# Optimization experiments

Hardware: AMD Instinct MI355X
Metric: run time of the kernel (lower is better)

## Reference

```python
import jax, jax.numpy as jnp
import numpy as np

B, T, D = 2, 2048, 1024
H = 16
HD = D // H  # 64


def setup_inputs() -> dict:
    key = jax.random.key(0)
    k1, k2, k3, k4, k5 = jax.random.split(key, 5)
    s = 0.02
    return {
        "x": jax.random.normal(k1, (B, T, D), dtype=jnp.float32),
        "Wqkv": jax.random.normal(k2, (D, 3 * D), dtype=jnp.float32) * s,
        "bqkv": jax.random.normal(k3, (3 * D,), dtype=jnp.float32) * s,
        "Wout": jax.random.normal(k4, (D, D), dtype=jnp.float32) * s,
        "bout": jax.random.normal(k5, (D,), dtype=jnp.float32) * s,
    }


def reference(x, Wqkv, bqkv, Wout, bout):
    b, t, c = x.shape
    qkv = (x @ Wqkv + bqkv).reshape(b, t, 3, H, HD)
    q = jnp.transpose(qkv[:, :, 0], (0, 2, 1, 3))  # [B,H,T,HD]
    k = jnp.transpose(qkv[:, :, 1], (0, 2, 1, 3))
    v = jnp.transpose(qkv[:, :, 2], (0, 2, 1, 3))
    att = jnp.einsum("bhqd,bhkd->bhqk", q, k) * (HD ** -0.5)
    mask = jnp.tril(jnp.ones((t, t), dtype=bool))  # causal, no past kv
    att = jnp.where(mask, att, -jnp.inf)
    att = jax.nn.softmax(att, axis=-1)
    y = jnp.einsum("bhqk,bhkd->bhqd", att, v)
    y = jnp.transpose(y, (0, 2, 1, 3)).reshape(b, t, c)
    return y @ Wout + bout
```

## Files before the change

kernel.cpp:

```cpp
#include <hip/hip_runtime.h>
#include <hip/hip_bf16.h>
#include <math.h>

#define B_  2
#define T_  2048
#define D_  1024
#define H_  16
#define HD_ 64

typedef __attribute__((ext_vector_type(8))) short short8;
typedef __attribute__((ext_vector_type(4))) float f32x4;
typedef __attribute__((ext_vector_type(4))) unsigned uint32x4;

#if __has_builtin(__builtin_amdgcn_exp2f)
#define EXP2F __builtin_amdgcn_exp2f
#else
#define EXP2F exp2f
#endif

__device__ __forceinline__ ushort f2bf(float x) {
    unsigned u = __builtin_bit_cast(unsigned, x);
    return (ushort)((u + 0x7FFFu + ((u >> 16) & 1u)) >> 16);
}

__device__ __forceinline__ unsigned pack_bf2_fast(float a, float b) {
    unsigned ua = __builtin_bit_cast(unsigned, a) + 0x8000u;
    unsigned ub = __builtin_bit_cast(unsigned, b) + 0x8000u;
    return (ua >> 16) | (ub & 0xFFFF0000u);
}

__device__ __forceinline__ void load_lds_16B(const ushort* g, ushort* l) {
    __builtin_amdgcn_global_load_lds(
        (const __attribute__((address_space(1))) unsigned*)g,
        (__attribute__((address_space(3))) unsigned*)l, 16, 0, 0);
}

__global__ __launch_bounds__(256)
void prep_kernel(const float* __restrict__ x, ushort* __restrict__ xb,
                 const float* __restrict__ Wqkv, ushort* __restrict__ Wqkvt,
                 const float* __restrict__ Wout, ushort* __restrict__ Woutt)
{
    __shared__ ushort Ts[64][65];
    const int bid = blockIdx.x;

    if (bid < 512) {
        const int n4 = (B_ * T_ * D_) / 4;
        for (int i = bid * 256 + threadIdx.x; i < n4; i += 512 * 256) {
            float4 v = ((const float4*)x)[i];
            ushort4 o = { f2bf(v.x), f2bf(v.y), f2bf(v.z), f2bf(v.w) };
            ((ushort4*)xb)[i] = o;
        }
        return;
    }

    const float* W; ushort* Wt; int K, M, m0, k0;
    if (bid < 1280) {
        const int t = bid - 512;
        W = Wqkv; Wt = Wqkvt; K = D_; M = 3 * D_;
        m0 = (t % 48) * 64; k0 = (t / 48) * 64;
    } else {
        const int t = bid - 1280;
        W = Wout; Wt = Woutt; K = D_; M = D_;
        m0 = (t % 16) * 64; k0 = (t / 16) * 64;
    }

    const int tr = threadIdx.x >> 4;
    const int tc = threadIdx.x & 15;
    #pragma unroll
    for (int it = 0; it < 4; it++) {
        int k = tr + it * 16;
        float4 v = *(const float4*)&W[(size_t)(k0 + k) * M + m0 + tc * 4];
        Ts[tc * 4 + 0][k] = f2bf(v.x);
        Ts[tc * 4 + 1][k] = f2bf(v.y);
        Ts[tc * 4 + 2][k] = f2bf(v.z);
        Ts[tc * 4 + 3][k] = f2bf(v.w);
    }
    __syncthreads();
    #pragma unroll
    for (int it = 0; it < 2; it++) {
        const int mr  = (threadIdx.x >> 3) + it * 32;
        const int seg = (threadIdx.x & 7) * 8;
        short8 v;
        #pragma unroll
        for (int r = 0; r < 8; r++) v[r] = (short)Ts[mr][seg + r];
        *(short8*)&Wt[(size_t)(m0 + mr) * K + k0 + seg] = v;
    }
}

__global__ __launch_bounds__(256, 4)
void gemm_qkv(const ushort* __restrict__ A, const ushort* __restrict__ Bt,
              const float* __restrict__ bias,
              ushort* __restrict__ Qg, ushort* __restrict__ Kg,
              ushort* __restrict__ Vtg)
{
    const int K = D_;
    __shared__ __align__(16) ushort lds[16384];
    ushort* Asl = lds;
    ushort* Bsl = lds + 8192;

    const int tid = threadIdx.x;
    const int w  = tid >> 6, L = tid & 63;
    const int lt = L & 15, lq = L >> 4;
    const int wr = w >> 1, wc = w & 1;
    const int m0 = blockIdx.x * 128, n0 = blockIdx.y * 128;
    const int rsub = L >> 3;
    const int pgr  = L & 7;

    f32x4 acc[4][4] = {};

    for (int k0 = 0; k0 < K; k0 += 64) {
        __syncthreads();
        #pragma unroll
        for (int j = 0; j < 4; j++) {
            const int row  = (w * 4 + j) * 8 + rsub;
            const int gran = pgr ^ rsub;
            load_lds_16B(A  + (size_t)(n0 + row) * K + k0 + gran * 8,
                         &Asl[row * 64 + pgr * 8]);
            load_lds_16B(Bt + (size_t)(m0 + row) * K + k0 + gran * 8,
                         &Bsl[row * 64 + pgr * 8]);
        }
        __syncthreads();

        #pragma unroll
        for (int ks = 0; ks < 2; ks++) {
            short8 af[4], bf[4];
            #pragma unroll
            for (int i = 0; i < 4; i++) {
                const int ra = wr * 64 + i * 16 + lt;
                af[i] = *(const short8*)&Asl[ra * 64 + (((ks * 4 + lq) ^ (ra & 7)) * 8)];
                const int rb = wc * 64 + i * 16 + lt;
                bf[i] = *(const short8*)&Bsl[rb * 64 + (((ks * 4 + lq) ^ (rb & 7)) * 8)];
            }
            #pragma unroll
            for (int i = 0; i < 4; i++)
                #pragma unroll
                for (int j = 0; j < 4; j++)
                    acc[i][j] = __builtin_amdgcn_mfma_f32_16x16x32_bf16(af[i], bf[j], acc[i][j], 0, 0, 0);
        }
    }

    __syncthreads();
    const int s  = m0 >> 10;
    const int h0 = (m0 & 1023) >> 6;
    const float qs = (s == 0) ? 0.18033688011112042f : 1.0f;

    if (s < 2) {
        #pragma unroll
        for (int j = 0; j < 4; j++) {
            const int m  = wc * 64 + j * 16 + lt;
            const float bv = bias[m0 + m];
            #pragma unroll
            for (int i = 0; i < 4; i++) {
                const int n = wr * 64 + i * 16 + lq * 4;
                #pragma unroll
                for (int r = 0; r < 4; r++)
                    lds[(n + r) * 128 + m] = f2bf((acc[i][j][r] + bv) * qs);
            }
        }
        __syncthreads();
        ushort* dst = (s == 0 ? Qg : Kg);
        #pragma unroll
        for (int it = 0; it < 8; it++) {
            const int g   = tid + it * 256;
            const int row = g >> 4, c = g & 15;
            const int n = n0 + row;
            const int b = n >> 11, t = n & 2047;
            const int h = h0 + (c >> 3), d = (c & 7) * 8;
            short8 v = *(const short8*)&lds[row * 128 + c * 8];
            *(short8*)&dst[((size_t)(b * H_ + h) * T_ + t) * HD_ + d] = v;
        }
    } else {
        #pragma unroll
        for (int j = 0; j < 4; j++) {
            const int m  = wc * 64 + j * 16 + lt;
            const float bv = bias[m0 + m];
            #pragma unroll
            for (int i = 0; i < 4; i++) {
                const int n = wr * 64 + i * 16 + lq * 4;
                uint2 pk = { pack_bf2_fast(acc[i][j][0] + bv, acc[i][j][1] + bv),
                             pack_bf2_fast(acc[i][j][2] + bv, acc[i][j][3] + bv) };
                *(uint2*)&lds[m * 128 + n] = pk;
            }
        }
        __syncthreads();
        const int b = n0 >> 11, t0 = n0 & 2047;
        #pragma unroll
        for (int it = 0; it < 8; it++) {
            const int g   = tid + it * 256;
            const int row = g >> 4, c = g & 15;
            const int h = h0 + (row >> 6), d = row & 63;
            short8 v = *(const short8*)&lds[row * 128 + c * 8];
            *(short8*)&Vtg[((size_t)(b * H_ + h) * HD_ + d) * T_ + t0 + c * 8] = v;
        }
    }
}

__global__ __launch_bounds__(256, 4)
void gemm_out(const ushort* __restrict__ A, const ushort* __restrict__ Bt,
              const float* __restrict__ bias, float* __restrict__ C)
{
    const int K = D_, M = D_;
    __shared__ __align__(16) ushort lds[8192 + 4096];
    ushort* Asl = lds;
    ushort* Bsl = lds + 8192;

    const int tid = threadIdx.x;
    const int w  = tid >> 6, L = tid & 63;
    const int lt = L & 15, lq = L >> 4;
    const int wr = w >> 1, wc = w & 1;
    const int m0 = blockIdx.x * 64, n0 = blockIdx.y * 128;
    const int rsub = L >> 3;
    const int pgr  = L & 7;

    f32x4 acc[2][4] = {};

    for (int k0 = 0; k0 < K; k0 += 64) {
        __syncthreads();
        #pragma unroll
        for (int j = 0; j < 4; j++) {
            const int row  = (w * 4 + j) * 8 + rsub;
            const int gran = pgr ^ rsub;
            load_lds_16B(A + (size_t)(n0 + row) * K + k0 + gran * 8,
                         &Asl[row * 64 + pgr * 8]);
        }
        #pragma unroll
        for (int j = 0; j < 2; j++) {
            const int row  = (w * 2 + j) * 8 + rsub;
            const int gran = pgr ^ rsub;
            load_lds_16B(Bt + (size_t)(m0 + row) * K + k0 + gran * 8,
                         &Bsl[row * 64 + pgr * 8]);
        }
        __syncthreads();

        #pragma unroll
        for (int ks = 0; ks < 2; ks++) {
            short8 wf[2], yf[4];
            #pragma unroll
            for (int j = 0; j < 2; j++) {
                const int rb = wc * 32 + j * 16 + lt;
                wf[j] = *(const short8*)&Bsl[rb * 64 + (((ks * 4 + lq) ^ (rb & 7)) * 8)];
            }
            #pragma unroll
            for (int i = 0; i < 4; i++) {
                const int ra = wr * 64 + i * 16 + lt;
                yf[i] = *(const short8*)&Asl[ra * 64 + (((ks * 4 + lq) ^ (ra & 7)) * 8)];
            }
            #pragma unroll
            for (int j = 0; j < 2; j++)
                #pragma unroll
                for (int i = 0; i < 4; i++)
                    acc[j][i] = __builtin_amdgcn_mfma_f32_16x16x32_bf16(wf[j], yf[i], acc[j][i], 0, 0, 0);
        }
    }

    #pragma unroll
    for (int j = 0; j < 2; j++) {
        const int mbase = m0 + wc * 32 + j * 16 + lq * 4;
        const float4 bv = *(const float4*)&bias[mbase];
        #pragma unroll
        for (int i = 0; i < 4; i++) {
            const int n = n0 + wr * 64 + i * 16 + lt;
            float4 o = { acc[j][i][0] + bv.x, acc[j][i][1] + bv.y,
                         acc[j][i][2] + bv.z, acc[j][i][3] + bv.w };
            *(float4*)&C[(size_t)n * M + mbase] = o;
        }
    }
}

__global__ __launch_bounds__(256, 4)
void attn_mfma(const ushort* __restrict__ Qg, const ushort* __restrict__ Kg,
               const ushort* __restrict__ Vtg, ushort* __restrict__ yb)
{
    const int h = blockIdx.y, b = blockIdx.z;
    const int flip = ((blockIdx.y >> 3) ^ blockIdx.z) & 1;
    const int qb = flip ? blockIdx.x : (31 - blockIdx.x);
    const int tid = threadIdx.x;
    const int w  = tid >> 6, L = tid & 63;
    const int lt = L & 15, lq = L >> 4;
    const int kswz = lt & 7;

    __shared__ __align__(16) ushort Ks [128 * 64];
    __shared__ __align__(16) ushort Vts[64 * 128];

    const size_t bh = (size_t)(b * H_ + h);
    const ushort* Qbase  = Qg  + bh * T_ * HD_;
    const ushort* Kbase  = Kg  + bh * T_ * HD_;
    const ushort* Vtbase = Vtg + bh * HD_ * T_;

    const int q_glob = qb * 64 + w * 16 + lt;
    const short8 qf0 = *(const short8*)(Qbase + (size_t)q_glob * HD_ + lq * 8);
    const short8 qf1 = *(const short8*)(Qbase + (size_t)q_glob * HD_ + 32 + lq * 8);

    f32x4 acc_o[4] = {};
    float lsum = 0.f;

    const int krow = tid >> 3, kpg = tid & 7;
    const int vrow = tid >> 4, vpg = tid & 15;
    const int nk = (qb + 2) >> 1;

    const int prow = ((lt >> 2) * 8) + (lt & 3);

    for (int kb = 0; kb < nk; kb++) {
        __syncthreads();
        #pragma unroll
        for (int rr = 0; rr < 4; rr++) {
            const int row = krow + 32 * rr;
            const int swzK = (((row >> 3) & 1) * 4) | (row & 3);
            load_lds_16B(Kbase + (size_t)(kb * 128 + row) * HD_ + (kpg ^ swzK) * 8,
                         &Ks[row * 64 + kpg * 8]);
        }
        #pragma unroll
        for (int rr = 0; rr < 4; rr++) {
            const int d = vrow + 16 * rr;
            load_lds_16B(Vtbase + (size_t)d * T_ + kb * 128 + (vpg ^ (d & 7)) * 8,
                         &Vts[d * 128 + vpg * 8]);
        }
        __syncthreads();

        if (kb < nk - 1) {
            short8 a00, a01, a10, a11, v0, v1, v2, v3;
            {
                const int row0 = prow, row1 = prow + 4;
                a00 = *(const short8*)&Ks[row0 * 64 + ((lq ^ kswz) * 8)];
                a01 = *(const short8*)&Ks[row0 * 64 + (((4 + lq) ^ kswz) * 8)];
                a10 = *(const short8*)&Ks[row1 * 64 + ((lq ^ kswz) * 8)];
                a11 = *(const short8*)&Ks[row1 * 64 + (((4 + lq) ^ kswz) * 8)];
                v0 = *(const short8*)&Vts[(0 * 16 + lt) * 128 + ((lq ^ kswz) * 8)];
                v1 = *(const short8*)&Vts[(1 * 16 + lt) * 128 + ((lq ^ kswz) * 8)];
                v2 = *(const short8*)&Vts[(2 * 16 + lt) * 128 + ((lq ^ kswz) * 8)];
                v3 = *(const short8*)&Vts[(3 * 16 + lt) * 128 + ((lq ^ kswz) * 8)];
            }
            #pragma unroll
            for (int ks = 0; ks < 4; ks++) {
                short8 b00, b01, b10, b11, w0, w1, w2, w3;
                if (ks < 3) {
                    const int row0 = (ks + 1) * 32 + prow, row1 = row0 + 4;
                    const int kc = ((ks + 1) * 4 + lq) ^ kswz;
                    b00 = *(const short8*)&Ks[row0 * 64 + ((lq ^ kswz) * 8)];
                    b01 = *(const short8*)&Ks[row0 * 64 + (((4 + lq) ^ kswz) * 8)];
                    b10 = *(const short8*)&Ks[row1 * 64 + ((lq ^ kswz) * 8)];
                    b11 = *(const short8*)&Ks[row1 * 64 + (((4 + lq) ^ kswz) * 8)];
                    w0 = *(const short8*)&Vts[(0 * 16 + lt) * 128 + (kc * 8)];
                    w1 = *(const short8*)&Vts[(1 * 16 + lt) * 128 + (kc * 8)];
                    w2 = *(const short8*)&Vts[(2 * 16 + lt) * 128 + (kc * 8)];
                    w3 = *(const short8*)&Vts[(3 * 16 + lt) * 128 + (kc * 8)];
                }
                f32x4 c0 = {}, c1 = {};
                c0 = __builtin_amdgcn_mfma_f32_16x16x32_bf16(a00, qf0, c0, 0, 0, 0);
                c0 = __builtin_amdgcn_mfma_f32_16x16x32_bf16(a01, qf1, c0, 0, 0, 0);
                c1 = __builtin_amdgcn_mfma_f32_16x16x32_bf16(a10, qf0, c1, 0, 0, 0);
                c1 = __builtin_amdgcn_mfma_f32_16x16x32_bf16(a11, qf1, c1, 0, 0, 0);

                float p[8];
                #pragma unroll
                for (int r = 0; r < 4; r++) { p[r] = EXP2F(c0[r]); p[4 + r] = EXP2F(c1[r]); }
                lsum += ((p[0] + p[1]) + (p[2] + p[3])) + ((p[4] + p[5]) + (p[6] + p[7]));

                uint32x4 pw = { pack_bf2_fast(p[0], p[1]), pack_bf2_fast(p[2], p[3]),
                                pack_bf2_fast(p[4], p[5]), pack_bf2_fast(p[6], p[7]) };
                short8 pf = __builtin_bit_cast(short8, pw);

                acc_o[0] = __builtin_amdgcn_mfma_f32_16x16x32_bf16(pf, v0, acc_o[0], 0, 0, 0);
                acc_o[1] = __builtin_amdgcn_mfma_f32_16x16x32_bf16(pf, v1, acc_o[1], 0, 0, 0);
                acc_o[2] = __builtin_amdgcn_mfma_f32_16x16x32_bf16(pf, v2, acc_o[2], 0, 0, 0);
                acc_o[3] = __builtin_amdgcn_mfma_f32_16x16x32_bf16(pf, v3, acc_o[3], 0, 0, 0);

                if (ks < 3) {
                    a00 = b00; a01 = b01; a10 = b10; a11 = b11;
                    v0 = w0; v1 = w1; v2 = w2; v3 = w3;
                }
            }
        } else {
            const int ksN = (qb & 1) ? 4 : 2;
            const int mk0 = (qb & 1) ? 2 : 0;
            for (int ks = 0; ks < ksN; ks++) {
                const int row0 = ks * 32 + prow;
                const int row1 = row0 + 4;
                short8 a00 = *(const short8*)&Ks[row0 * 64 + ((lq ^ kswz) * 8)];
                short8 a01 = *(const short8*)&Ks[row0 * 64 + (((4 + lq) ^ kswz) * 8)];
                short8 a10 = *(const short8*)&Ks[row1 * 64 + ((lq ^ kswz) * 8)];
                short8 a11 = *(const short8*)&Ks[row1 * 64 + (((4 + lq) ^ kswz) * 8)];
                f32x4 c0 = {}, c1 = {};
                c0 = __builtin_amdgcn_mfma_f32_16x16x32_bf16(a00, qf0, c0, 0, 0, 0);
                c0 = __builtin_amdgcn_mfma_f32_16x16x32_bf16(a01, qf1, c0, 0, 0, 0);
                c1 = __builtin_amdgcn_mfma_f32_16x16x32_bf16(a10, qf0, c1, 0, 0, 0);
                c1 = __builtin_amdgcn_mfma_f32_16x16x32_bf16(a11, qf1, c1, 0, 0, 0);

                float p[8];
                #pragma unroll
                for (int r = 0; r < 4; r++) { p[r] = EXP2F(c0[r]); p[4 + r] = EXP2F(c1[r]); }
                if (ks >= mk0) {
                    const int key0 = kb * 128 + ks * 32 + lq * 8;
                    #pragma unroll
                    for (int r = 0; r < 4; r++) {
                        if (key0 + r > q_glob)     p[r]     = 0.f;
                        if (key0 + 4 + r > q_glob) p[4 + r] = 0.f;
                    }
                }
                lsum += ((p[0] + p[1]) + (p[2] + p[3])) + ((p[4] + p[5]) + (p[6] + p[7]));

                uint32x4 pw = { pack_bf2_fast(p[0], p[1]), pack_bf2_fast(p[2], p[3]),
                                pack_bf2_fast(p[4], p[5]), pack_bf2_fast(p[6], p[7]) };
                short8 pf = __builtin_bit_cast(short8, pw);

                #pragma unroll
                for (int dt = 0; dt < 4; dt++) {
                    const int vr = dt * 16 + lt;
                    short8 vf = *(const short8*)&Vts[vr * 128 + (((ks * 4 + lq) ^ kswz) * 8)];
                    acc_o[dt] = __builtin_amdgcn_mfma_f32_16x16x32_bf16(pf, vf, acc_o[dt], 0, 0, 0);
                }
            }
        }
    }

    lsum += __shfl_xor(lsum, 16, 64);
    lsum += __shfl_xor(lsum, 32, 64);
    const float inv = 1.0f / lsum;

    float linv[4];
    #pragma unroll
    for (int r = 0; r < 4; r++) linv[r] = __shfl(inv, lq * 4 + r, 64);

    ushort* ybase = yb + (size_t)(b * T_ + qb * 64 + w * 16) * D_ + h * HD_;
    #pragma unroll
    for (int r = 0; r < 4; r++)
        #pragma unroll
        for (int dt = 0; dt < 4; dt++)
            ybase[(size_t)(lq * 4 + r) * D_ + dt * 16 + lt] = f2bf(acc_o[dt][r] * linv[r]);
}

extern "C" void kernel_launch(void* const* d_in, const int* in_sizes, int n_in,
                              void* d_out, int out_size, void* d_ws, size_t ws_size,
                              hipStream_t stream)
{
    const float* x    = (const float*)d_in[0];
    const float* Wqkv = (const float*)d_in[1];
    const float* bqkv = (const float*)d_in[2];
    const float* Wout = (const float*)d_in[3];
    const float* bout = (const float*)d_in[4];
    float* out = (float*)d_out;

    char* ws = (char*)d_ws;
    const size_t NT = (size_t)B_ * T_;
    ushort* xb     = (ushort*)ws;
    ushort* Wqkvt  = (ushort*)(ws + NT * D_ * 2);
    ushort* Woutt  = (ushort*)(ws + NT * D_ * 2 + (size_t)3 * D_ * D_ * 2);
    char*   p      = ws + NT * D_ * 2 + (size_t)4 * D_ * D_ * 2;
    const size_t qkv_elems = (size_t)B_ * H_ * T_ * HD_;
    ushort* Qg  = (ushort*)p;
    ushort* Kg  = (ushort*)(p + qkv_elems * 2);
    ushort* Vtg = (ushort*)(p + qkv_elems * 4);
    ushort* yb  = (ushort*)(p + qkv_elems * 6);

    prep_kernel<<<1536, 256, 0, stream>>>(x, xb, Wqkv, Wqkvt, Wout, Woutt);

    gemm_qkv<<<dim3(3 * D_ / 128, NT / 128), 256, 0, stream>>>(
        xb, Wqkvt, bqkv, Qg, Kg, Vtg);

    attn_mfma<<<dim3(32, H_, B_), 256, 0, stream>>>(Qg, Kg, Vtg, yb);

    gemm_out<<<dim3(D_ / 64, NT / 128), 256, 0, stream>>>(
        yb, Woutt, bout, out);
}
```

Before: 166.9 us.

## Enlarge QKV GEMM tile to 256x256 with double-buffered LDS prefetch

The QKV projection GEMM moves from 128x128 tiles on 256 threads to 256x256 tiles on 512 threads. Global-to-LDS loads are now double-buffered: the next K-slice loads while the current one is computed, with explicit vmcnt waits and barriers. This aims to raise data reuse per tile and hide global load latency. In exchange it uses 128KB of LDS per block, allows only one block per CU, and launches just 12x16=192 blocks, which may underfill the 256 CUs.

```diff
diff --git a/kernel.cpp b/kernel.cpp
--- a/kernel.cpp
+++ b/kernel.cpp
@@ -87,59 +87,78 @@
     }
 }
 
-__global__ __launch_bounds__(256, 4)
+__global__ __launch_bounds__(512, 1)
 void gemm_qkv(const ushort* __restrict__ A, const ushort* __restrict__ Bt,
               const float* __restrict__ bias,
               ushort* __restrict__ Qg, ushort* __restrict__ Kg,
               ushort* __restrict__ Vtg)
 {
-    const int K = D_;
-    __shared__ __align__(16) ushort lds[16384];
-    ushort* Asl = lds;
-    ushort* Bsl = lds + 8192;
+    __shared__ __align__(16) ushort lds[65536];
 
     const int tid = threadIdx.x;
     const int w  = tid >> 6, L = tid & 63;
     const int lt = L & 15, lq = L >> 4;
-    const int wr = w >> 1, wc = w & 1;
-    const int m0 = blockIdx.x * 128, n0 = blockIdx.y * 128;
+    const int wr = w >> 2;
+    const int wc = w & 3;
+    const int m0 = blockIdx.x * 256, n0 = blockIdx.y * 256;
     const int rsub = L >> 3;
     const int pgr  = L & 7;
 
-    f32x4 acc[4][4] = {};
-
-    for (int k0 = 0; k0 < K; k0 += 64) {
-        __syncthreads();
+    f32x4 acc[8][4] = {};
+
+    auto STAGE = [&](int t, int buf) {
+        ushort* Asl = lds + buf * 16384;
+        ushort* Bsl = lds + 32768 + buf * 16384;
+        const int k0 = t * 64;
         #pragma unroll
         for (int j = 0; j < 4; j++) {
-            const int row  = (w * 4 + j) * 8 + rsub;
+            const int row  = w * 32 + j * 8 + rsub;
             const int gran = pgr ^ rsub;
-            load_lds_16B(A  + (size_t)(n0 + row) * K + k0 + gran * 8,
+            load_lds_16B(A  + (size_t)(n0 + row) * D_ + k0 + gran * 8,
                          &Asl[row * 64 + pgr * 8]);
-            load_lds_16B(Bt + (size_t)(m0 + row) * K + k0 + gran * 8,
+            load_lds_16B(Bt + (size_t)(m0 + row) * D_ + k0 + gran * 8,
                          &Bsl[row * 64 + pgr * 8]);
         }
-        __syncthreads();
-
+    };
+
+    STAGE(0, 0);
+    STAGE(1, 1);
+    int cur = 0;
+
+    for (int t = 0; t < 16; t++) {
+        if (t < 15) asm volatile("s_waitcnt vmcnt(8)" ::: "memory");
+        else        asm volatile("s_waitcnt vmcnt(0)" ::: "memory");
+        __builtin_amdgcn_s_barrier();
+        __builtin_amdgcn_sched_barrier(0);
+
+        const ushort* Asl = lds + cur * 16384;
+        const ushort* Bsl = lds + 32768 + cur * 16384;
         #pragma unroll
         for (int ks = 0; ks < 2; ks++) {
-            short8 af[4], bf[4];
-            #pragma unroll
-            for (int i = 0; i < 4; i++) {
-                const int ra = wr * 64 + i * 16 + lt;
+            short8 af[8], bf[4];
+            #pragma unroll
+            for (int i = 0; i < 8; i++) {
+                const int ra = wr * 128 + i * 16 + lt;
                 af[i] = *(const short8*)&Asl[ra * 64 + (((ks * 4 + lq) ^ (ra & 7)) * 8)];
-                const int rb = wc * 64 + i * 16 + lt;
-                bf[i] = *(const short8*)&Bsl[rb * 64 + (((ks * 4 + lq) ^ (rb & 7)) * 8)];
-            }
-            #pragma unroll
-            for (int i = 0; i < 4; i++)
+            }
+            #pragma unroll
+            for (int j = 0; j < 4; j++) {
+                const int rb = wc * 64 + j * 16 + lt;
+                bf[j] = *(const short8*)&Bsl[rb * 64 + (((ks * 4 + lq) ^ (rb & 7)) * 8)];
+            }
+            #pragma unroll
+            for (int i = 0; i < 8; i++)
                 #pragma unroll
                 for (int j = 0; j < 4; j++)
                     acc[i][j] = __builtin_amdgcn_mfma_f32_16x16x32_bf16(af[i], bf[j], acc[i][j], 0, 0, 0);
         }
-    }
-
-    __syncthreads();
+
+        __builtin_amdgcn_s_barrier();
+        __builtin_amdgcn_sched_barrier(0);
+        if (t + 2 < 16) STAGE(t + 2, cur);
+        cur ^= 1;
+    }
+
     const int s  = m0 >> 10;
     const int h0 = (m0 & 1023) >> 6;
     const float qs = (s == 0) ? 0.18033688011112042f : 1.0f;
@@ -150,24 +169,24 @@
             const int m  = wc * 64 + j * 16 + lt;
             const float bv = bias[m0 + m];
             #pragma unroll
-            for (int i = 0; i < 4; i++) {
-                const int n = wr * 64 + i * 16 + lq * 4;
+            for (int i = 0; i < 8; i++) {
+                const int n = wr * 128 + i * 16 + lq * 4;
                 #pragma unroll
                 for (int r = 0; r < 4; r++)
-                    lds[(n + r) * 128 + m] = f2bf((acc[i][j][r] + bv) * qs);
+                    lds[(n + r) * 256 + m] = f2bf((acc[i][j][r] + bv) * qs);
             }
         }
         __syncthreads();
         ushort* dst = (s == 0 ? Qg : Kg);
         #pragma unroll
-        for (int it = 0; it < 8; it++) {
-            const int g   = tid + it * 256;
-            const int row = g >> 4, c = g & 15;
+        for (int it = 0; it < 16; it++) {
+            const int g   = tid + it * 512;
+            const int row = g >> 5, c = g & 31;
             const int n = n0 + row;
-            const int b = n >> 11, t = n & 2047;
+            const int b = n >> 11, tq = n & 2047;
             const int h = h0 + (c >> 3), d = (c & 7) * 8;
-            short8 v = *(const short8*)&lds[row * 128 + c * 8];
-            *(short8*)&dst[((size_t)(b * H_ + h) * T_ + t) * HD_ + d] = v;
+            short8 v = *(const short8*)&lds[row * 256 + c * 8];
+            *(short8*)&dst[((size_t)(b * H_ + h) * T_ + tq) * HD_ + d] = v;
         }
     } else {
         #pragma unroll
@@ -175,21 +194,21 @@
             const int m  = wc * 64 + j * 16 + lt;
             const float bv = bias[m0 + m];
             #pragma unroll
-            for (int i = 0; i < 4; i++) {
-                const int n = wr * 64 + i * 16 + lq * 4;
+            for (int i = 0; i < 8; i++) {
+                const int n = wr * 128 + i * 16 + lq * 4;
                 uint2 pk = { pack_bf2_fast(acc[i][j][0] + bv, acc[i][j][1] + bv),
                              pack_bf2_fast(acc[i][j][2] + bv, acc[i][j][3] + bv) };
-                *(uint2*)&lds[m * 128 + n] = pk;
+                *(uint2*)&lds[m * 256 + n] = pk;
             }
         }
         __syncthreads();
         const int b = n0 >> 11, t0 = n0 & 2047;
         #pragma unroll
-        for (int it = 0; it < 8; it++) {
-            const int g   = tid + it * 256;
-            const int row = g >> 4, c = g & 15;
+        for (int it = 0; it < 16; it++) {
+            const int g   = tid + it * 512;
+            const int row = g >> 5, c = g & 31;
             const int h = h0 + (row >> 6), d = row & 63;
-            short8 v = *(const short8*)&lds[row * 128 + c * 8];
+            short8 v = *(const short8*)&lds[row * 256 + c * 8];
             *(short8*)&Vtg[((size_t)(b * H_ + h) * HD_ + d) * T_ + t0 + c * 8] = v;
         }
     }
@@ -454,7 +473,7 @@
 
     prep_kernel<<<1536, 256, 0, stream>>>(x, xb, Wqkv, Wqkvt, Wout, Woutt);
 
-    gemm_qkv<<<dim3(3 * D_ / 128, NT / 128), 256, 0, stream>>>(
+    gemm_qkv<<<dim3(3 * D_ / 256, NT / 256), 512, 0, stream>>>(
         xb, Wqkvt, bqkv, Qg, Kg, Vtg);
 
     attn_mfma<<<dim3(32, H_, B_), 256, 0, stream>>>(Qg, Kg, Vtg, yb);
```

After: 174.7 us. 4.7% more time.
